# Kernel optimization log

Measured on AMD Instinct MI355X. Metric: run time of the kernel, lower is better.

Reference implementation:

```python
import jax, jax.numpy as jnp
import numpy as np

B, CHAR_LEN, LSTM, VOCAB, NATTN = 4096, 64, 400, 73, 10

def _lstm_cell(x, h, c, W_ih, W_hh, b):
    # gates: [B, 4*LSTM] in (i, f, g, o) order, matching torch.nn.LSTMCell
    g = x @ W_ih.T + h @ W_hh.T + b
    i, f, gg, o = jnp.split(g, 4, axis=1)
    i = jax.nn.sigmoid(i); f = jax.nn.sigmoid(f)
    gg = jnp.tanh(gg); o = jax.nn.sigmoid(o)
    c_new = f * c + i * gg
    h_new = o * jnp.tanh(c_new)
    return h_new, c_new

def setup_inputs() -> dict:
    key = jax.random.key(0)
    ks = jax.random.split(key, 24)
    d = {}
    d['inputs'] = jax.random.normal(ks[0], (B, 3), jnp.float32)
    for n, k in zip(['h1','c1','h2','c2','h3','c3'], ks[1:7]):
        d[n] = jax.random.normal(k, (B, LSTM), jnp.float32) * 0.1
    d['kappa'] = jax.random.uniform(ks[7], (B, NATTN), jnp.float32) * 5.0
    d['w_prev'] = jax.random.uniform(ks[8], (B, VOCAB), jnp.float32)
    d['attention_values'] = jax.random.uniform(ks[9], (B, CHAR_LEN, VOCAB), jnp.float32)
    d['attention_lengths'] = jax.random.randint(ks[10], (B,), 1, CHAR_LEN + 1, jnp.int32)
    s = 0.05
    in1 = VOCAB + 3              # lstm1 input: [w, inputs]
    in23 = 3 + LSTM + VOCAB      # lstm2/3 input: [inputs, h, w]
    attn_in = VOCAB + 3 + LSTM
    d['W_ih1'] = jax.random.normal(ks[11], (4 * LSTM, in1), jnp.float32) * s
    d['W_hh1'] = jax.random.normal(ks[12], (4 * LSTM, LSTM), jnp.float32) * s
    d['b1'] = jax.random.normal(ks[13], (4 * LSTM,), jnp.float32) * s
    d['W_attn'] = jax.random.normal(ks[14], (3 * NATTN, attn_in), jnp.float32) * s
    d['b_attn'] = jax.random.normal(ks[15], (3 * NATTN,), jnp.float32) * s
    d['W_ih2'] = jax.random.normal(ks[16], (4 * LSTM, in23), jnp.float32) * s
    d['W_hh2'] = jax.random.normal(ks[17], (4 * LSTM, LSTM), jnp.float32) * s
    d['b2'] = jax.random.normal(ks[18], (4 * LSTM,), jnp.float32) * s
    d['W_ih3'] = jax.random.normal(ks[19], (4 * LSTM, in23), jnp.float32) * s
    d['W_hh3'] = jax.random.normal(ks[20], (4 * LSTM, LSTM), jnp.float32) * s
    d['b3'] = jax.random.normal(ks[21], (4 * LSTM,), jnp.float32) * s
    return d

def reference(inputs, h1, c1, h2, c2, h3, c3, kappa, w_prev, attention_values,
              attention_lengths, W_ih1, W_hh1, b1, W_attn, b_attn,
              W_ih2, W_hh2, b2, W_ih3, W_hh3, b3):
    char_len = attention_values.shape[1]
    # --- LSTM 1 ---
    s1_in = jnp.concatenate([w_prev, inputs], axis=1)
    h1n, c1n = _lstm_cell(s1_in, h1, c1, W_ih1, W_hh1, b1)
    # --- Gaussian-mixture location attention ---
    attn_in = jnp.concatenate([w_prev, inputs, h1n], axis=1)
    attn_params = jax.nn.softplus(attn_in @ W_attn.T + b_attn)
    alpha, beta, kap = jnp.split(attn_params, 3, axis=1)
    kap = kappa + kap / 25.0
    beta = jnp.maximum(beta, 0.01)
    u = jnp.arange(char_len, dtype=jnp.float32)[None, None, :]           # [1,1,C]
    phi = jnp.sum(alpha[:, :, None] *
                  jnp.exp(-jnp.square(kap[:, :, None] - u) / beta[:, :, None]),
                  axis=1)                                                 # [B,C]
    seq_mask = (jnp.arange(char_len)[None, :] < attention_lengths[:, None]).astype(jnp.float32)
    w = jnp.einsum('bc,bcv->bv', phi * seq_mask, attention_values)        # [B,V]
    # --- LSTM 2 & 3 ---
    s2_in = jnp.concatenate([inputs, h1n, w], axis=1)
    h2n, c2n = _lstm_cell(s2_in, h2, c2, W_ih2, W_hh2, b2)
    s3_in = jnp.concatenate([inputs, h2n, w], axis=1)
    h3n, c3n = _lstm_cell(s3_in, h3, c3, W_ih3, W_hh3, b3)
    return h3n
```

## Files before the change

### kernel.cpp

```cpp
#include <hip/hip_runtime.h>
#include <hip/hip_bf16.h>


#define B_SZ     4096
#define LSTM_N   400
#define NG       1600
#define VOCAB    73
#define NATTN    10
#define CHARLEN  64
#define KP1      512
#define KP23     896

typedef _Float16 half8 __attribute__((ext_vector_type(8)));
typedef __attribute__((ext_vector_type(4))) float floatx4;

__device__ __forceinline__ void gload_lds16(const void* g, void* l) {
    __builtin_amdgcn_global_load_lds(
        (const __attribute__((address_space(1))) void*)g,
        (__attribute__((address_space(3))) void*)l, 16, 0, 0);
}

__device__ __forceinline__ int lds_off(int r, int g) {
    return (r << 6) + ((((g ^ r) & 7)) << 3);
}

#define CW1   102400
#define CW23  179200
#define CWA   4096
#define CX1   262144
#define CXA   57344
#define CX23  253952
#define O1    (CW1)
#define O2    (O1 + CW23)
#define O3    (O2 + CW23)
#define O4    (O3 + CWA)
#define O5    (O4 + CX1)
#define O6    (O5 + CXA)
#define O7    (O6 + CX23)

__global__ __launch_bounds__(256) void pack_all(const float* __restrict__ Wih1,
                                                const float* __restrict__ Whh1,
                                                const float* __restrict__ Wih2,
                                                const float* __restrict__ Whh2,
                                                const float* __restrict__ Wih3,
                                                const float* __restrict__ Whh3,
                                                const float* __restrict__ W_attn,
                                                const float* __restrict__ w_prev,
                                                const float* __restrict__ inputs,
                                                const float* __restrict__ h1,
                                                const float* __restrict__ h2,
                                                const float* __restrict__ h3,
                                                _Float16* __restrict__ W1,
                                                _Float16* __restrict__ W2,
                                                _Float16* __restrict__ W3,
                                                _Float16* __restrict__ Wa,
                                                _Float16* __restrict__ X1,
                                                _Float16* __restrict__ XA,
                                                _Float16* __restrict__ X2,
                                                _Float16* __restrict__ X3)
{
    const int id = blockIdx.x * 256 + threadIdx.x;
    half8 hv;

    if (id < O1) {
        const int row = id >> 6;
        const int k0  = (id & 63) << 3;
        const int u = row >> 2, g = row & 3;
        const int src = g * 400 + u;
#pragma unroll
        for (int e = 0; e < 8; e++) {
            const int k = k0 + e;
            float x = 0.f;
            if (k < 76)           x = Wih1[(size_t)src * 76 + k];
            else if (k < 476)     x = Whh1[(size_t)src * 400 + (k - 76)];
            hv[e] = (_Float16)x;
        }
        *(half8*)(W1 + (size_t)row * KP1 + k0) = hv;
    } else if (id < O3) {
        const int id2 = id - O1;
        const bool is3 = (id2 >= CW23);
        const int id3 = is3 ? id2 - CW23 : id2;
        const int row = id3 / 112;
        const int k0  = (id3 - row * 112) << 3;
        const int u = row >> 2, g = row & 3;
        const int src = g * 400 + u;
        const float* Wih = is3 ? Wih3 : Wih2;
        const float* Whh = is3 ? Whh3 : Whh2;
#pragma unroll
        for (int e = 0; e < 8; e++) {
            const int k = k0 + e;
            float x = 0.f;
            if (k < 400)          x = Wih[(size_t)src * 476 + 3 + k];
            else if (k < 403)     x = Wih[(size_t)src * 476 + (k - 400)];
            else if (k < 476)     x = Wih[(size_t)src * 476 + k];
            else if (k < 876)     x = Whh[(size_t)src * 400 + (k - 476)];
            hv[e] = (_Float16)x;
        }
        *(half8*)((is3 ? W3 : W2) + (size_t)row * KP23 + k0) = hv;
    } else if (id < O4) {
        const int id4 = id - O3;
        const int row = id4 >> 6;
        const int k0  = (id4 & 63) << 3;
#pragma unroll
        for (int e = 0; e < 8; e++) {
            const int k = k0 + e;
            float x = 0.f;
            if (row < 30) {
                if (k < 400)      x = W_attn[(size_t)row * 476 + 76 + k];
                else if (k < 473) x = W_attn[(size_t)row * 476 + (k - 400)];
                else if (k < 476) x = W_attn[(size_t)row * 476 + 73 + (k - 473)];
            }
            hv[e] = (_Float16)x;
        }
        *(half8*)(Wa + (size_t)row * KP1 + k0) = hv;
    } else if (id < O5) {
        const int id5 = id - O4;
        const int b  = id5 >> 6;
        const int k0 = (id5 & 63) << 3;
#pragma unroll
        for (int e = 0; e < 8; e++) {
            const int k = k0 + e;
            float x = 0.f;
            if (k < 73)           x = w_prev[(size_t)b * 73 + k];
            else if (k < 76)      x = inputs[(size_t)b * 3 + (k - 73)];
            else if (k < 476)     x = h1[(size_t)b * 400 + (k - 76)];
            hv[e] = (_Float16)x;
        }
        *(half8*)(X1 + (size_t)b * KP1 + k0) = hv;
    } else if (id < O6) {
        const int id6 = id - O5;
        const int b  = id6 / 14;
        const int k0 = 400 + ((id6 - b * 14) << 3);
#pragma unroll
        for (int e = 0; e < 8; e++) {
            const int k = k0 + e;
            float x = 0.f;
            if (k < 473)          x = w_prev[(size_t)b * 73 + (k - 400)];
            else if (k < 476)     x = inputs[(size_t)b * 3 + (k - 473)];
            hv[e] = (_Float16)x;
        }
        *(half8*)(XA + (size_t)b * KP1 + k0) = hv;
    } else if (id < O7) {
        const int id7 = id - O6;
        const int b  = id7 / 62;
        const int k0 = 400 + ((id7 - b * 62) << 3);
        half8 h2v, h3v;
#pragma unroll
        for (int e = 0; e < 8; e++) {
            const int k = k0 + e;
            float x2 = 0.f, x3 = 0.f;
            if (k < 403)                    { x2 = inputs[(size_t)b * 3 + (k - 400)]; x3 = x2; }
            else if (k >= 476 && k < 876)   { x2 = h2[(size_t)b * 400 + (k - 476)];
                                              x3 = h3[(size_t)b * 400 + (k - 476)]; }
            h2v[e] = (_Float16)x2;
            h3v[e] = (_Float16)x3;
        }
        *(half8*)(X2 + (size_t)b * KP23 + k0) = h2v;
        *(half8*)(X3 + (size_t)b * KP23 + k0) = h3v;
    }
}

template<int KP>
__global__ __launch_bounds__(512, 6) void gemm_fused_t(const _Float16* __restrict__ Wm,
                                                       const _Float16* __restrict__ X,
                                                       const float* __restrict__ bias,
                                                       const float* __restrict__ c_in,
                                                       _Float16* __restrict__ d1, int ld1,
                                                       _Float16* __restrict__ d2, int ld2,
                                                       float* __restrict__ fout)
{
    __shared__ _Float16 lds[2][192 * 64];

    const int t    = threadIdx.x;
    const int w    = t >> 6;
    const int lane = t & 63;
    const int quad = lane >> 4;
    const int l16  = lane & 15;
    const int fid  = blockIdx.y * 32 + blockIdx.x;
    const int xcd  = fid & 7;
    const int loc  = fid >> 3;
    const int bx   = xcd * 4 + loc / 25;
    const int by   = loc % 25;
    const int m0   = by * 64;
    const int n0   = bx * 128;
    const int wm   = (w >> 2) * 32;
    const int wn   = (w & 3) * 32;
    const int lr   = lane >> 3;
    const int gq   = (lane & 7) ^ lr;

    floatx4 acc[2][2] = {};

    auto stage = [&](int sb, int k0) {
        gload_lds16(Wm + (size_t)(m0 + w * 8 + lr) * KP + k0 + gq * 8,
                    &lds[sb][(w * 8) * 64]);
#pragma unroll
        for (int s = 0; s < 2; s++) {
            const int c = w * 2 + s;
            gload_lds16(X + (size_t)(n0 + c * 8 + lr) * KP + k0 + gq * 8,
                        &lds[sb][(64 + c * 8) * 64]);
        }
    };

    stage(0, 0);
    constexpr int NT = KP / 64;
#pragma unroll
    for (int kt = 0; kt < NT; kt++) {
        const int sb = kt & 1;
        if (kt + 1 < NT) {
            stage(sb ^ 1, (kt + 1) * 64);
            asm volatile("s_waitcnt vmcnt(3)" ::: "memory");
        } else {
            asm volatile("s_waitcnt vmcnt(0)" ::: "memory");
        }
        __builtin_amdgcn_s_barrier();
        __builtin_amdgcn_sched_barrier(0);

#pragma unroll
        for (int h = 0; h < 2; h++) {
            half8 af[2], bf[2];
#pragma unroll
            for (int i = 0; i < 2; i++)
                af[i] = *(const half8*)(&lds[sb][lds_off(wm + i * 16 + l16, h * 4 + quad)]);
#pragma unroll
            for (int i = 0; i < 2; i++)
                bf[i] = *(const half8*)(&lds[sb][lds_off(64 + wn + i * 16 + l16, h * 4 + quad)]);
            __builtin_amdgcn_s_setprio(1);
#pragma unroll
            for (int mt = 0; mt < 2; mt++)
#pragma unroll
                for (int nt = 0; nt < 2; nt++)
                    acc[mt][nt] = __builtin_amdgcn_mfma_f32_16x16x32_f16(
                        af[mt], bf[nt], acc[mt][nt], 0, 0, 0);
            __builtin_amdgcn_s_setprio(0);
        }
        __builtin_amdgcn_s_barrier();
    }
    __builtin_amdgcn_sched_barrier(0);

    const int u0 = m0 >> 2;
    float*    Cs   = (float*)&lds[0][0];
    _Float16* Hs16 = (_Float16*)&lds[1][0];
    float*    Hs32 = (float*)&lds[1][0];
    {
        const int bl = t >> 2;
        const int p  = t & 3;
        floatx4 cv = *(const floatx4*)(c_in + (size_t)(n0 + bl) * LSTM_N + u0 + p * 4);
        *(floatx4*)(Cs + bl * 20 + p * 4) = cv;
    }
    __syncthreads();

#pragma unroll
    for (int mt = 0; mt < 2; mt++) {
        const int ul = (wm >> 2) + mt * 4 + quad;
        const int u  = u0 + ul;
        const float bi  = bias[u];
        const float bff = bias[400 + u];
        const float bg  = bias[800 + u];
        const float bo  = bias[1200 + u];
#pragma unroll
        for (int nt = 0; nt < 2; nt++) {
            const int bl = wn + nt * 16 + l16;
            float gi = acc[mt][nt][0] + bi;
            float gf = acc[mt][nt][1] + bff;
            float gg = acc[mt][nt][2] + bg;
            float go = acc[mt][nt][3] + bo;
            float si = 1.f / (1.f + expf(-gi));
            float sf = 1.f / (1.f + expf(-gf));
            float so = 1.f / (1.f + expf(-go));
            float cn = sf * Cs[bl * 20 + ul] + si * tanhf(gg);
            float h  = so * tanhf(cn);
            if (fout) Hs32[bl * 20 + ul] = h;
            else      Hs16[bl * 24 + ul] = (_Float16)h;
        }
    }
    __syncthreads();

    if (fout) {
        const int bl = t >> 2;
        const int ch = t & 3;
        *(floatx4*)(fout + (size_t)(n0 + bl) * LSTM_N + u0 + ch * 4) =
            *(const floatx4*)(Hs32 + bl * 20 + ch * 4);
    } else if (t < 256) {
        const int bl = t >> 1;
        const int p  = t & 1;
        half8 hvv = *(const half8*)(Hs16 + bl * 24 + p * 8);
        *(half8*)(d1 + (size_t)(n0 + bl) * ld1 + u0 + p * 8) = hvv;
        if (d2) *(half8*)(d2 + (size_t)(n0 + bl) * ld2 + u0 + p * 8) = hvv;
    }
}

__global__ __launch_bounds__(256) void attn_fused(const _Float16* __restrict__ Wa,
                                                  const _Float16* __restrict__ XA,
                                                  const float* __restrict__ b_attn,
                                                  const float* __restrict__ kappa,
                                                  const float* __restrict__ AV,
                                                  const int* __restrict__ alen,
                                                  _Float16* __restrict__ X2,
                                                  _Float16* __restrict__ X3)
{
    __shared__ _Float16 Wa_s[30 * KP1];
    __shared__ float prm[4][32];
    __shared__ float phi_s[4][CHARLEN];

    const int t = threadIdx.x;
#pragma unroll
    for (int i = 0; i < 8; i++) {
        const int idx = t + i * 256;
        if (idx < 1920) {
            const int row = idx >> 6;
            const int c8  = (idx & 63) << 3;
            *(half8*)(&Wa_s[row * KP1 + c8]) = *(const half8*)(Wa + (size_t)row * KP1 + c8);
        }
    }
    __syncthreads();

    const int wave = t >> 6;
    const int lane = t & 63;
    const int b = blockIdx.x * 4 + wave;

    half8 xa = *(const half8*)(XA + (size_t)b * KP1 + lane * 8);
    float xf[8];
#pragma unroll
    for (int e = 0; e < 8; e++) xf[e] = (float)xa[e];

    float myp = 0.f;
#pragma unroll
    for (int m = 0; m < 30; m++) {
        half8 wv = *(const half8*)(&Wa_s[m * KP1 + lane * 8]);
        float s = 0.f;
#pragma unroll
        for (int e = 0; e < 8; e++) s += (float)wv[e] * xf[e];
#pragma unroll
        for (int sh = 32; sh >= 1; sh >>= 1) s += __shfl_xor(s, sh, 64);
        if (lane == m) myp = s;
    }

    if (lane < 30) {
        float p  = myp + b_attn[lane];
        float sp = (p > 20.f) ? p : log1pf(expf(p));
        float v;
        if (lane < 10)      v = sp;
        else if (lane < 20) v = fmaxf(sp, 0.01f);
        else                v = kappa[(size_t)b * NATTN + (lane - 20)] + sp * (1.f / 25.f);
        prm[wave][lane] = v;
    }
    __syncthreads();

    const int len = alen[b];
    {
        int c = lane;
        float phi = 0.f;
#pragma unroll
        for (int j = 0; j < NATTN; j++) {
            float d = prm[wave][20 + j] - (float)c;
            phi += prm[wave][j] * expf(-d * d / prm[wave][10 + j]);
        }
        phi_s[wave][c] = (c < len) ? phi : 0.f;
    }
    __syncthreads();

    for (int v0 = 0; v0 < VOCAB; v0 += 64) {
        const int v = v0 + lane;
        if (v < VOCAB) {
            const float* avb = AV + (size_t)b * CHARLEN * VOCAB + v;
            float s = 0.f;
            for (int c = 0; c < len; c++)
                s += phi_s[wave][c] * avb[(size_t)c * VOCAB];
            _Float16 wv = (_Float16)s;
            X2[(size_t)b * KP23 + 403 + v] = wv;
            X3[(size_t)b * KP23 + 403 + v] = wv;
        }
    }
}

extern "C" void kernel_launch(void* const* d_in, const int* in_sizes, int n_in,
                              void* d_out, int out_size, void* d_ws, size_t ws_size,
                              hipStream_t stream)
{
    const float* inputs = (const float*)d_in[0];
    const float* h1     = (const float*)d_in[1];
    const float* c1     = (const float*)d_in[2];
    const float* h2     = (const float*)d_in[3];
    const float* c2     = (const float*)d_in[4];
    const float* h3     = (const float*)d_in[5];
    const float* c3     = (const float*)d_in[6];
    const float* kappa  = (const float*)d_in[7];
    const float* w_prev = (const float*)d_in[8];
    const float* AV     = (const float*)d_in[9];
    const int*   alen   = (const int*)d_in[10];
    const float* W_ih1  = (const float*)d_in[11];
    const float* W_hh1  = (const float*)d_in[12];
    const float* b1     = (const float*)d_in[13];
    const float* W_attn = (const float*)d_in[14];
    const float* b_attn = (const float*)d_in[15];
    const float* W_ih2  = (const float*)d_in[16];
    const float* W_hh2  = (const float*)d_in[17];
    const float* b2     = (const float*)d_in[18];
    const float* W_ih3  = (const float*)d_in[19];
    const float* W_hh3  = (const float*)d_in[20];
    const float* b3     = (const float*)d_in[21];
    float* out = (float*)d_out;

    char* p = (char*)d_ws;
    _Float16* X1 = (_Float16*)p; p += (size_t)B_SZ * KP1 * 2;
    _Float16* XA = (_Float16*)p; p += (size_t)B_SZ * KP1 * 2;
    _Float16* X2 = (_Float16*)p; p += (size_t)B_SZ * KP23 * 2;
    _Float16* X3 = (_Float16*)p; p += (size_t)B_SZ * KP23 * 2;
    _Float16* W1 = (_Float16*)p; p += (size_t)NG * KP1 * 2;
    _Float16* W2 = (_Float16*)p; p += (size_t)NG * KP23 * 2;
    _Float16* W3 = (_Float16*)p; p += (size_t)NG * KP23 * 2;
    _Float16* Wa = (_Float16*)p; p += (size_t)64 * KP1 * 2;

    pack_all<<<O7 / 256, 256, 0, stream>>>(W_ih1, W_hh1, W_ih2, W_hh2,
                                           W_ih3, W_hh3, W_attn,
                                           w_prev, inputs, h1, h2, h3,
                                           W1, W2, W3, Wa, X1, XA, X2, X3);

    const dim3 fgrid(32, 25);

    gemm_fused_t<KP1><<<fgrid, 512, 0, stream>>>(W1, X1, b1, c1,
                                                 XA, KP1, X2, KP23, nullptr);
    attn_fused<<<B_SZ / 4, 256, 0, stream>>>(Wa, XA, b_attn, kappa, AV, alen, X2, X3);
    gemm_fused_t<KP23><<<fgrid, 512, 0, stream>>>(W2, X2, b2, c2,
                                                  X3, KP23, nullptr, 0, nullptr);
    gemm_fused_t<KP23><<<fgrid, 512, 0, stream>>>(W3, X3, b3, c3,
                                                  nullptr, 0, nullptr, 0, out);
}
```

Before: 278.7 us.

## Enlarge fused LSTM GEMM tile to 128x128 with 1024 threads and padded M

Changes the fused gate GEMM from 64x128 tiles with 512 threads to 128x128 tiles with 1024 threads (16 waves). The gate dimension is padded from 1600 to 1664 rows so it divides into 13 tiles, with zero rows in the packed weights and guards in the epilogue for the partial last tile. The goal is fewer blocks and more reuse of each activation tile loaded into LDS. In exchange, about 4% of the MFMA work is wasted on padding rows, and the larger blocks raise LDS use per block and reduce occupancy flexibility.

```diff
diff --git a/kernel.cpp b/kernel.cpp
--- a/kernel.cpp
+++ b/kernel.cpp
@@ -4,7 +4,8 @@
 
 #define B_SZ     4096
 #define LSTM_N   400
-#define NG       1600
+#define MPAD     1664
+#define MT       13
 #define VOCAB    73
 #define NATTN    10
 #define CHARLEN  64
@@ -24,8 +25,8 @@
     return (r << 6) + ((((g ^ r) & 7)) << 3);
 }
 
-#define CW1   102400
-#define CW23  179200
+#define CW1   106496
+#define CW23  186368
 #define CWA   4096
 #define CX1   262144
 #define CXA   57344
@@ -71,8 +72,10 @@
         for (int e = 0; e < 8; e++) {
             const int k = k0 + e;
             float x = 0.f;
-            if (k < 76)           x = Wih1[(size_t)src * 76 + k];
-            else if (k < 476)     x = Whh1[(size_t)src * 400 + (k - 76)];
+            if (u < 400) {
+                if (k < 76)           x = Wih1[(size_t)src * 76 + k];
+                else if (k < 476)     x = Whh1[(size_t)src * 400 + (k - 76)];
+            }
             hv[e] = (_Float16)x;
         }
         *(half8*)(W1 + (size_t)row * KP1 + k0) = hv;
@@ -90,10 +93,12 @@
         for (int e = 0; e < 8; e++) {
             const int k = k0 + e;
             float x = 0.f;
-            if (k < 400)          x = Wih[(size_t)src * 476 + 3 + k];
-            else if (k < 403)     x = Wih[(size_t)src * 476 + (k - 400)];
-            else if (k < 476)     x = Wih[(size_t)src * 476 + k];
-            else if (k < 876)     x = Whh[(size_t)src * 400 + (k - 476)];
+            if (u < 400) {
+                if (k < 400)          x = Wih[(size_t)src * 476 + 3 + k];
+                else if (k < 403)     x = Wih[(size_t)src * 476 + (k - 400)];
+                else if (k < 476)     x = Wih[(size_t)src * 476 + k];
+                else if (k < 876)     x = Whh[(size_t)src * 400 + (k - 476)];
+            }
             hv[e] = (_Float16)x;
         }
         *(half8*)((is3 ? W3 : W2) + (size_t)row * KP23 + k0) = hv;
@@ -161,15 +166,15 @@
 }
 
 template<int KP>
-__global__ __launch_bounds__(512, 6) void gemm_fused_t(const _Float16* __restrict__ Wm,
-                                                       const _Float16* __restrict__ X,
-                                                       const float* __restrict__ bias,
-                                                       const float* __restrict__ c_in,
-                                                       _Float16* __restrict__ d1, int ld1,
-                                                       _Float16* __restrict__ d2, int ld2,
-                                                       float* __restrict__ fout)
+__global__ __launch_bounds__(1024, 8) void gemm_fused_t(const _Float16* __restrict__ Wm,
+                                                        const _Float16* __restrict__ X,
+                                                        const float* __restrict__ bias,
+                                                        const float* __restrict__ c_in,
+                                                        _Float16* __restrict__ d1, int ld1,
+                                                        _Float16* __restrict__ d2, int ld2,
+                                                        float* __restrict__ fout)
 {
-    __shared__ _Float16 lds[2][192 * 64];
+    __shared__ _Float16 lds[2][256 * 64];
 
     const int t    = threadIdx.x;
     const int w    = t >> 6;
@@ -179,9 +184,9 @@
     const int fid  = blockIdx.y * 32 + blockIdx.x;
     const int xcd  = fid & 7;
     const int loc  = fid >> 3;
-    const int bx   = xcd * 4 + loc / 25;
-    const int by   = loc % 25;
-    const int m0   = by * 64;
+    const int bx   = xcd * 4 + loc / 13;
+    const int by   = loc % 13;
+    const int m0   = by * 128;
     const int n0   = bx * 128;
     const int wm   = (w >> 2) * 32;
     const int wn   = (w & 3) * 32;
@@ -193,12 +198,8 @@
     auto stage = [&](int sb, int k0) {
         gload_lds16(Wm + (size_t)(m0 + w * 8 + lr) * KP + k0 + gq * 8,
                     &lds[sb][(w * 8) * 64]);
-#pragma unroll
-        for (int s = 0; s < 2; s++) {
-            const int c = w * 2 + s;
-            gload_lds16(X + (size_t)(n0 + c * 8 + lr) * KP + k0 + gq * 8,
-                        &lds[sb][(64 + c * 8) * 64]);
-        }
+        gload_lds16(X + (size_t)(n0 + w * 8 + lr) * KP + k0 + gq * 8,
+                    &lds[sb][(128 + w * 8) * 64]);
     };
 
     stage(0, 0);
@@ -208,7 +209,7 @@
         const int sb = kt & 1;
         if (kt + 1 < NT) {
             stage(sb ^ 1, (kt + 1) * 64);
-            asm volatile("s_waitcnt vmcnt(3)" ::: "memory");
+            asm volatile("s_waitcnt vmcnt(2)" ::: "memory");
         } else {
             asm volatile("s_waitcnt vmcnt(0)" ::: "memory");
         }
@@ -223,7 +224,7 @@
                 af[i] = *(const half8*)(&lds[sb][lds_off(wm + i * 16 + l16, h * 4 + quad)]);
 #pragma unroll
             for (int i = 0; i < 2; i++)
-                bf[i] = *(const half8*)(&lds[sb][lds_off(64 + wn + i * 16 + l16, h * 4 + quad)]);
+                bf[i] = *(const half8*)(&lds[sb][lds_off(128 + wn + i * 16 + l16, h * 4 + quad)]);
             __builtin_amdgcn_s_setprio(1);
 #pragma unroll
             for (int mt = 0; mt < 2; mt++)
@@ -237,15 +238,18 @@
     }
     __builtin_amdgcn_sched_barrier(0);
 
-    const int u0 = m0 >> 2;
+    const int u0     = by * 32;
+    const int nvalid = (u0 + 32 <= LSTM_N) ? 32 : (LSTM_N - u0);
     float*    Cs   = (float*)&lds[0][0];
     _Float16* Hs16 = (_Float16*)&lds[1][0];
     float*    Hs32 = (float*)&lds[1][0];
     {
-        const int bl = t >> 2;
-        const int p  = t & 3;
-        floatx4 cv = *(const floatx4*)(c_in + (size_t)(n0 + bl) * LSTM_N + u0 + p * 4);
-        *(floatx4*)(Cs + bl * 20 + p * 4) = cv;
+        const int bl = t >> 3;
+        const int p  = t & 7;
+        if (p * 4 < nvalid) {
+            floatx4 cv = *(const floatx4*)(c_in + (size_t)(n0 + bl) * LSTM_N + u0 + p * 4);
+            *(floatx4*)(Cs + bl * 36 + p * 4) = cv;
+        }
     }
     __syncthreads();
 
@@ -253,10 +257,11 @@
     for (int mt = 0; mt < 2; mt++) {
         const int ul = (wm >> 2) + mt * 4 + quad;
         const int u  = u0 + ul;
-        const float bi  = bias[u];
-        const float bff = bias[400 + u];
-        const float bg  = bias[800 + u];
-        const float bo  = bias[1200 + u];
+        const bool uv = ul < nvalid;
+        const float bi  = uv ? bias[u] : 0.f;
+        const float bff = uv ? bias[400 + u] : 0.f;
+        const float bg  = uv ? bias[800 + u] : 0.f;
+        const float bo  = uv ? bias[1200 + u] : 0.f;
 #pragma unroll
         for (int nt = 0; nt < 2; nt++) {
             const int bl = wn + nt * 16 + l16;
@@ -267,25 +272,30 @@
             float si = 1.f / (1.f + expf(-gi));
             float sf = 1.f / (1.f + expf(-gf));
             float so = 1.f / (1.f + expf(-go));
-            float cn = sf * Cs[bl * 20 + ul] + si * tanhf(gg);
+            float cn = sf * (uv ? Cs[bl * 36 + ul] : 0.f) + si * tanhf(gg);
             float h  = so * tanhf(cn);
-            if (fout) Hs32[bl * 20 + ul] = h;
-            else      Hs16[bl * 24 + ul] = (_Float16)h;
+            if (uv) {
+                if (fout) Hs32[bl * 36 + ul] = h;
+                else      Hs16[bl * 40 + ul] = (_Float16)h;
+            }
         }
     }
     __syncthreads();
 
     if (fout) {
+        const int bl = t >> 3;
+        const int ch = t & 7;
+        if (ch * 4 < nvalid)
+            *(floatx4*)(fout + (size_t)(n0 + bl) * LSTM_N + u0 + ch * 4) =
+                *(const floatx4*)(Hs32 + bl * 36 + ch * 4);
+    } else if (t < 512) {
         const int bl = t >> 2;
         const int ch = t & 3;
-        *(floatx4*)(fout + (size_t)(n0 + bl) * LSTM_N + u0 + ch * 4) =
-            *(const floatx4*)(Hs32 + bl * 20 + ch * 4);
-    } else if (t < 256) {
-        const int bl = t >> 1;
-        const int p  = t & 1;
-        half8 hvv = *(const half8*)(Hs16 + bl * 24 + p * 8);
-        *(half8*)(d1 + (size_t)(n0 + bl) * ld1 + u0 + p * 8) = hvv;
-        if (d2) *(half8*)(d2 + (size_t)(n0 + bl) * ld2 + u0 + p * 8) = hvv;
+        if (ch * 8 < nvalid) {
+            half8 hvv = *(const half8*)(Hs16 + bl * 40 + ch * 8);
+            *(half8*)(d1 + (size_t)(n0 + bl) * ld1 + u0 + ch * 8) = hvv;
+            if (d2) *(half8*)(d2 + (size_t)(n0 + bl) * ld2 + u0 + ch * 8) = hvv;
+        }
     }
 }
 
@@ -406,9 +416,9 @@
     _Float16* XA = (_Float16*)p; p += (size_t)B_SZ * KP1 * 2;
     _Float16* X2 = (_Float16*)p; p += (size_t)B_SZ * KP23 * 2;
     _Float16* X3 = (_Float16*)p; p += (size_t)B_SZ * KP23 * 2;
-    _Float16* W1 = (_Float16*)p; p += (size_t)NG * KP1 * 2;
-    _Float16* W2 = (_Float16*)p; p += (size_t)NG * KP23 * 2;
-    _Float16* W3 = (_Float16*)p; p += (size_t)NG * KP23 * 2;
+    _Float16* W1 = (_Float16*)p; p += (size_t)MPAD * KP1 * 2;
+    _Float16* W2 = (_Float16*)p; p += (size_t)MPAD * KP23 * 2;
+    _Float16* W3 = (_Float16*)p; p += (size_t)MPAD * KP23 * 2;
     _Float16* Wa = (_Float16*)p; p += (size_t)64 * KP1 * 2;
 
     pack_all<<<O7 / 256, 256, 0, stream>>>(W_ih1, W_hh1, W_ih2, W_hh2,
@@ -416,13 +426,13 @@
                                            w_prev, inputs, h1, h2, h3,
                                            W1, W2, W3, Wa, X1, XA, X2, X3);
 
-    const dim3 fgrid(32, 25);
-
-    gemm_fused_t<KP1><<<fgrid, 512, 0, stream>>>(W1, X1, b1, c1,
-                                                 XA, KP1, X2, KP23, nullptr);
+    const dim3 fgrid(32, MT);
+
+    gemm_fused_t<KP1><<<fgrid, 1024, 0, stream>>>(W1, X1, b1, c1,
+                                                  XA, KP1, X2, KP23, nullptr);
     attn_fused<<<B_SZ / 4, 256, 0, stream>>>(Wa, XA, b_attn, kappa, AV, alen, X2, X3);
-    gemm_fused_t<KP23><<<fgrid, 512, 0, stream>>>(W2, X2, b2, c2,
-                                                  X3, KP23, nullptr, 0, nullptr);
-    gemm_fused_t<KP23><<<fgrid, 512, 0, stream>>>(W3, X3, b3, c3,
-                                                  nullptr, 0, nullptr, 0, out);
-}
+    gemm_fused_t<KP23><<<fgrid, 1024, 0, stream>>>(W2, X2, b2, c2,
+                                                   X3, KP23, nullptr, 0, nullptr);
+    gemm_fused_t<KP23><<<fgrid, 1024, 0, stream>>>(W3, X3, b3, c3,
+                                                   nullptr, 0, nullptr, 0, out);
+}
```

After: 279.5 us. No clear change (+0.3%).
